# Kernel tuning notes

Hardware: AMD Instinct MI355X
Metric: run time of the kernel (lower is better)

Reference implementation:

```python
import jax, jax.numpy as jnp
import numpy as np

HEADS = 4
DIM_HEAD = 128


def setup_inputs() -> dict:
    key = jax.random.key(0)
    k1, k2, k3, k4 = jax.random.split(key, 4)
    b, dim, H, W = 4, 256, 128, 128
    hidden = HEADS * DIM_HEAD  # 512
    x = jax.random.normal(k1, (b, dim, H, W), dtype=jnp.float32)
    # 1x1 convs are pointwise matmuls over channels
    w_qkv = jax.random.normal(k2, (hidden * 3, dim), dtype=jnp.float32) * 0.02
    w_out = jax.random.normal(k3, (dim, hidden), dtype=jnp.float32) * 0.02
    b_out = jax.random.normal(k4, (dim,), dtype=jnp.float32) * 0.02
    return {"x": x, "w_qkv": w_qkv, "w_out": w_out, "b_out": b_out}


def reference(x, w_qkv, w_out, b_out):
    b, c, h, w = x.shape
    n = h * w
    # to_qkv: 1x1 conv (no bias) == channel matmul -> [b, 3*heads*dh, h, w]
    qkv = jnp.einsum('bchw,oc->bohw', x, w_qkv)
    # 'b (qkv heads d) h w -> qkv b heads d (h w)'
    qkv = qkv.reshape(b, 3, HEADS, DIM_HEAD, n)
    q, k, v = qkv[:, 0], qkv[:, 1], qkv[:, 2]  # each [b, heads, d, n]
    k = jax.nn.softmax(k, axis=-1)  # softmax over spatial positions
    context = jnp.einsum('bhdn,bhen->bhde', k, v)   # [b, heads, d, d]
    out = jnp.einsum('bhde,bhdn->bhen', context, q)  # [b, heads, d, n]
    out = out.reshape(b, HEADS * DIM_HEAD, h, w)
    # to_out: 1x1 conv with bias
    return jnp.einsum('bchw,oc->bohw', out, w_out) + b_out[None, :, None, None]
```

## Files before the change

kernel.cpp:

```cpp
#include <hip/hip_runtime.h>
#include <hip/hip_bf16.h>

#define HEADS 4
#define DH    128
#define CIN   256
#define NPIX  16384
#define NB    4
#define HID   512

typedef __attribute__((ext_vector_type(8))) short bf16x8;
typedef __attribute__((ext_vector_type(4))) float f32x4;
typedef __attribute__((ext_vector_type(2))) unsigned u32x2;

__device__ __forceinline__ unsigned short f2bfu(float f) {
    union { __hip_bfloat16 h; unsigned short u; } cv;
    cv.h = __float2bfloat16(f);
    return cv.u;
}

typedef const __attribute__((address_space(1))) unsigned char* gas_t;
typedef __attribute__((address_space(3))) unsigned char* las_t;
__device__ __forceinline__ void glds16(const void* g, void* s) {
    __builtin_amdgcn_global_load_lds((gas_t)g, (las_t)s, 16, 0, 0);
}
__device__ __forceinline__ unsigned lds_off(const void* p) {
    return (unsigned)(size_t)(las_t)p;
}


__global__ __launch_bounds__(256) void xp_convert(const float* __restrict__ x,
                                                  unsigned short* __restrict__ xp)
{
    __shared__ float tile[64][67];
    const int b = blockIdx.z, c0 = blockIdx.y * 64, n0 = blockIdx.x * 64;
    const int t = threadIdx.x;
    const float* xb = x + ((size_t)b * CIN + c0) * NPIX + n0;
#pragma unroll
    for (int p = 0; p < 4; ++p) {
        const int c = p * 16 + (t >> 4);
        const int n = (t & 15) * 4;
        float4 v = *reinterpret_cast<const float4*>(xb + (size_t)c * NPIX + n);
        tile[c][n + 0] = v.x; tile[c][n + 1] = v.y;
        tile[c][n + 2] = v.z; tile[c][n + 3] = v.w;
    }
    __syncthreads();
    const int n16l = t >> 6, c16l = (t >> 4) & 3, n_loc = t & 15;
    unsigned short u16[16];
#pragma unroll
    for (int j = 0; j < 16; ++j)
        u16[j] = f2bfu(tile[c16l * 16 + j][n16l * 16 + n_loc]);
    unsigned short* dst = xp + (((size_t)(b * 1024 + (n0 >> 4) + n16l)) * 16
                                + (c0 >> 4) + c16l) * 256 + n_loc * 16;
    *reinterpret_cast<uint4*>(dst)     = *reinterpret_cast<const uint4*>(u16);
    *reinterpret_cast<uint4*>(dst + 8) = *reinterpret_cast<const uint4*>(u16 + 8);
}

__global__ __launch_bounds__(256) void wconv3(const float* __restrict__ w_qkv,
                                              const float* __restrict__ w_out,
                                              unsigned short* __restrict__ WkF,
                                              unsigned short* __restrict__ WvF,
                                              unsigned short* __restrict__ WqTF,
                                              unsigned short* __restrict__ WoF)
{
    const int t = threadIdx.x, lane = t & 63, wid = t >> 6;
    const int tile = blockIdx.x * 4 + wid;
    unsigned short u8[8];
    unsigned short* dst;
    if (tile < 256) {
        const int h = tile >> 6, d16 = (tile >> 3) & 7, c32 = tile & 7;
        const float* src = w_qkv + (size_t)(512 + h * 128 + d16 * 16 + (lane & 15)) * CIN
                         + c32 * 32 + (lane >> 4) * 8;
#pragma unroll
        for (int j = 0; j < 8; ++j) u8[j] = f2bfu(src[j]);
        dst = WkF + (size_t)tile * 512 + lane * 8;
    } else if (tile < 512) {
        const int t2 = tile - 256;
        const int h = t2 >> 6, e16 = (t2 >> 3) & 7, c32 = t2 & 7;
        const float* src = w_qkv + (size_t)(1024 + h * 128 + e16 * 16 + (lane & 15)) * CIN
                         + c32 * 32 + (lane >> 4) * 8;
#pragma unroll
        for (int j = 0; j < 8; ++j) u8[j] = f2bfu(src[j]);
        dst = WvF + (size_t)t2 * 512 + lane * 8;
    } else if (tile < 768) {
        const int t2 = tile - 512;
        const int h = t2 >> 6, c16 = (t2 >> 2) & 15, d32 = t2 & 3;
#pragma unroll
        for (int j = 0; j < 8; ++j)
            u8[j] = f2bfu(w_qkv[(size_t)(h * 128 + d32 * 32 + (lane >> 4) * 8 + j) * CIN
                                + c16 * 16 + (lane & 15)]);
        dst = WqTF + (size_t)t2 * 512 + lane * 8;
    } else {
        const int t2 = tile - 768;
        const int o16 = t2 >> 4, m32 = t2 & 15;
        const float* src = w_out + (size_t)(o16 * 16 + (lane & 15)) * HID
                         + m32 * 32 + (lane >> 4) * 8;
#pragma unroll
        for (int j = 0; j < 8; ++j) u8[j] = f2bfu(src[j]);
        dst = WoF + (size_t)t2 * 512 + lane * 8;
    }
    *reinterpret_cast<uint4*>(dst) = *reinterpret_cast<const uint4*>(u8);
}

__global__ __launch_bounds__(512, 2) void kg_fused7(const unsigned short* __restrict__ xp,
                                                    const unsigned short* __restrict__ WkF,
                                                    float* __restrict__ Gp,
                                                    float* __restrict__ S)
{
    __shared__ unsigned short sX[2][64 * 256];
    __shared__ unsigned short sP[16 * 512];

    const int wgid = blockIdx.x;
    const int xcd  = wgid & 7;
    const int k_   = wgid >> 3;
    const int h    = k_ & 3;
    const int g_   = xcd + 8 * (k_ >> 2);
    const int ns   = g_ & 15;
    const int b    = g_ >> 4;
    const int bh   = b * 4 + h;

    const int t = threadIdx.x, lane = t & 63, wid = t >> 6;
    const int wm = wid >> 1, wn = wid & 1;
    const int wd = wid >> 2, wcq = wid & 3;
    const int cl = lane & 15, q = lane >> 4, r0q = q * 4;
    const int boff  = cl * 16 + (q & 1) * 8 + (q >> 1) * 256;
    const unsigned troff = (unsigned)((q >> 1) * 8192 + (q & 1) * 256 + cl * 8);

    bf16x8 aW[2][8];
#pragma unroll
    for (int fi = 0; fi < 2; ++fi)
#pragma unroll
        for (int ks = 0; ks < 8; ++ks)
            aW[fi][ks] = *reinterpret_cast<const bf16x8*>(
                WkF + ((size_t)(h * 64 + (wm * 2 + fi) * 8 + ks)) * 512 + lane * 8);

    f32x4 accG[4][4] = {};
    float Sacc[8] = {};

    const unsigned short* xpb = xp + ((size_t)(b * 1024 + ns * 64) * 16) * 256;

#define STAGE(nt_, buf_)                                                        \
    {                                                                           \
        const unsigned short* src_ = xpb + (size_t)(nt_) * 16384;               \
        _Pragma("unroll")                                                       \
        for (int p = 0; p < 4; ++p)                                             \
            glds16(src_ + ((size_t)p * 512 + t) * 8,                            \
                   &sX[buf_][((size_t)p * 512 + wid * 64) * 8]);                \
    }

    STAGE(0, 0);
    __syncthreads();

    int cur = 0;
    for (int nt = 0; nt < 16; ++nt) {
        if (nt < 15) STAGE(nt + 1, cur ^ 1);

        f32x4 acc1[2][2] = {};
#pragma unroll
        for (int ks = 0; ks < 8; ++ks) {
            bf16x8 bb[2];
#pragma unroll
            for (int fj = 0; fj < 2; ++fj)
                bb[fj] = *reinterpret_cast<const bf16x8*>(
                    &sX[cur][((wn * 2 + fj) * 16 + 2 * ks) * 256 + boff]);
#pragma unroll
            for (int fi = 0; fi < 2; ++fi)
#pragma unroll
                for (int fj = 0; fj < 2; ++fj)
                    acc1[fi][fj] = __builtin_amdgcn_mfma_f32_16x16x32_bf16(
                        aW[fi][ks], bb[fj], acc1[fi][fj], 0, 0, 0);
        }

#pragma unroll
        for (int fi = 0; fi < 2; ++fi)
#pragma unroll
            for (int r = 0; r < 4; ++r) {
                float rs = 0.f;
#pragma unroll
                for (int fj = 0; fj < 2; ++fj) {
                    const float v = __expf(acc1[fi][fj][r]);
                    rs += v;
                    const int us = ((r0q + r) + 16 * (fj * 2 + (cl >> 3))) * 8 + (cl & 7);
                    sP[((wm * 2 + fi) * 2 + wn) * 512 + us] = f2bfu(v);
                }
                Sacc[fi * 4 + r] += rs;
            }
        __syncthreads();

        {
            const unsigned sx_base = lds_off(&sX[cur][0]);
#pragma unroll
            for (int kn = 0; kn < 2; ++kn) {
                u32x2 lo[4], hi[4];
#pragma unroll
                for (int fj = 0; fj < 4; ++fj) {
                    const int cc = wcq * 4 + fj;
                    const unsigned a = sx_base + (unsigned)((kn * 32 + cc) * 512) + troff;
                    asm volatile("ds_read_b64_tr_b16 %0, %2\n\t"
                                 "ds_read_b64_tr_b16 %1, %2 offset:128"
                                 : "=&v"(lo[fj]), "=&v"(hi[fj])
                                 : "v"(a));
                }
                asm volatile("s_waitcnt lgkmcnt(0)" ::: "memory");
                __builtin_amdgcn_sched_barrier(0);

                bf16x8 pa[4];
#pragma unroll
                for (int fi = 0; fi < 4; ++fi)
                    pa[fi] = *reinterpret_cast<const bf16x8*>(
                        &sP[((wd * 4 + fi) * 2 + kn) * 512 + lane * 8]);
#pragma unroll
                for (int fj = 0; fj < 4; ++fj) {
                    union { bf16x8 v; u32x2 h2[2]; } fb;
                    fb.h2[0] = lo[fj];
                    fb.h2[1] = hi[fj];
#pragma unroll
                    for (int fi = 0; fi < 4; ++fi)
                        accG[fi][fj] = __builtin_amdgcn_mfma_f32_16x16x32_bf16(
                            pa[fi], fb.v, accG[fi][fj], 0, 0, 0);
                }
            }
        }
        __syncthreads();
        cur ^= 1;
    }
#undef STAGE

#pragma unroll
    for (int i = 0; i < 8; ++i) {
        float v = Sacc[i];
        v += __shfl_xor(v, 1); v += __shfl_xor(v, 2);
        v += __shfl_xor(v, 4); v += __shfl_xor(v, 8);
        if (cl == 0) {
            const int d = wm * 32 + (i >> 2) * 16 + r0q + (i & 3);
            atomicAdd(&S[bh * 128 + d], v);
        }
    }

    float* gp = Gp + (size_t)(ns * 16 + bh) * (128 * 256);
#pragma unroll
    for (int fi = 0; fi < 4; ++fi)
#pragma unroll
        for (int fj = 0; fj < 4; ++fj)
#pragma unroll
            for (int r = 0; r < 4; ++r)
                gp[(size_t)(wd * 64 + fi * 16 + r0q + r) * 256 + wcq * 64 + fj * 16 + cl]
                    = accG[fi][fj][r];
}

__global__ __launch_bounds__(256) void g_reduce2(const float* __restrict__ Gp,
                                                 float* __restrict__ G)
{
    const int idx = blockIdx.x * 256 + threadIdx.x;
    const int bh = idx >> 15, dc = idx & 32767;
    float s = 0.f;
#pragma unroll
    for (int k = 0; k < 16; ++k)
        s += Gp[((size_t)k * 16 + bh) * 32768 + dc];
    G[idx] = s;
}

__global__ __launch_bounds__(256) void c1_kernel(const float* __restrict__ G,
                                                 const float* __restrict__ S,
                                                 const unsigned short* __restrict__ WvF,
                                                 const unsigned short* __restrict__ WqTF,
                                                 unsigned short* __restrict__ AbarF)
{
    __shared__ unsigned short sCtx[32 * 512];
    const int t = threadIdx.x, lane = t & 63, wid = t >> 6;
    const int bh = blockIdx.x, b = bh >> 2, h = bh & 3;
    const int cl = lane & 15, r0q = (lane >> 4) * 4;
    const int wr = wid >> 1, wc = wid & 1;
    const float* Gb = G + (size_t)bh * 32768;

    float invs[4];
#pragma unroll
    for (int fi = 0; fi < 4; ++fi)
        invs[fi] = 1.0f / S[bh * 128 + wr * 64 + fi * 16 + cl];

    f32x4 acc[4][4] = {};
#pragma unroll
    for (int ks = 0; ks < 8; ++ks) {
        bf16x8 a[4], bb[4];
#pragma unroll
        for (int fi = 0; fi < 4; ++fi) {
            const float* gp = Gb + (size_t)(wr * 64 + fi * 16 + cl) * 256
                            + ks * 32 + (lane >> 4) * 8;
            const float4 v0 = *reinterpret_cast<const float4*>(gp);
            const float4 v1 = *reinterpret_cast<const float4*>(gp + 4);
            unsigned short u8[8] = {
                f2bfu(v0.x * invs[fi]), f2bfu(v0.y * invs[fi]),
                f2bfu(v0.z * invs[fi]), f2bfu(v0.w * invs[fi]),
                f2bfu(v1.x * invs[fi]), f2bfu(v1.y * invs[fi]),
                f2bfu(v1.z * invs[fi]), f2bfu(v1.w * invs[fi]) };
            a[fi] = *reinterpret_cast<const bf16x8*>(u8);
        }
#pragma unroll
        for (int fj = 0; fj < 4; ++fj)
            bb[fj] = *reinterpret_cast<const bf16x8*>(
                WvF + ((size_t)(h * 8 + wc * 4 + fj) * 8 + ks) * 512 + lane * 8);
#pragma unroll
        for (int fi = 0; fi < 4; ++fi)
#pragma unroll
            for (int fj = 0; fj < 4; ++fj)
                acc[fi][fj] = __builtin_amdgcn_mfma_f32_16x16x32_bf16(
                    a[fi], bb[fj], acc[fi][fj], 0, 0, 0);
    }

#pragma unroll
    for (int fi = 0; fi < 4; ++fi)
#pragma unroll
        for (int fj = 0; fj < 4; ++fj)
#pragma unroll
            for (int r = 0; r < 4; ++r) {
                const int us = (cl + 16 * ((fi & 1) * 2 + ((r0q + r) >> 3))) * 8 + ((r0q + r) & 7);
                sCtx[((wc * 4 + fj) * 4 + wr * 2 + (fi >> 1)) * 512 + us] = f2bfu(acc[fi][fj][r]);
            }
    __syncthreads();

    const int we = wid >> 1, wcq = wid & 1;
    f32x4 acc2[4][8] = {};
#pragma unroll
    for (int ks = 0; ks < 4; ++ks) {
        bf16x8 a2[4], b2[8];
#pragma unroll
        for (int fi = 0; fi < 4; ++fi)
            a2[fi] = *reinterpret_cast<const bf16x8*>(
                &sCtx[((we * 4 + fi) * 4 + ks) * 512 + lane * 8]);
#pragma unroll
        for (int fj = 0; fj < 8; ++fj)
            b2[fj] = *reinterpret_cast<const bf16x8*>(
                WqTF + ((size_t)(h * 16 + wcq * 8 + fj) * 4 + ks) * 512 + lane * 8);
#pragma unroll
        for (int fi = 0; fi < 4; ++fi)
#pragma unroll
            for (int fj = 0; fj < 8; ++fj)
                acc2[fi][fj] = __builtin_amdgcn_mfma_f32_16x16x32_bf16(
                    a2[fi], b2[fj], acc2[fi][fj], 0, 0, 0);
    }

#pragma unroll
    for (int fi = 0; fi < 4; ++fi)
#pragma unroll
        for (int fj = 0; fj < 8; ++fj)
#pragma unroll
            for (int r = 0; r < 4; ++r) {
                const int c16 = wcq * 8 + fj;
                const int m32 = h * 4 + we * 2 + (fi >> 1);
                const int us  = (cl + 16 * ((fi & 1) * 2 + ((r0q + r) >> 3))) * 8 + ((r0q + r) & 7);
                AbarF[((size_t)(b * 16 + c16) * 16 + m32) * 512 + us] = f2bfu(acc2[fi][fj][r]);
            }
}

__global__ __launch_bounds__(256) void c2_kernel(const unsigned short* __restrict__ WoF,
                                                 const unsigned short* __restrict__ AbarF,
                                                 unsigned short* __restrict__ F2)
{
    const int t = threadIdx.x, lane = t & 63, wid = t >> 6;
    const int csp = blockIdx.x, b = blockIdx.y;
    const int cl = lane & 15, r0q = (lane >> 4) * 4;

    f32x4 acc[4][4] = {};
#pragma unroll
    for (int ks = 0; ks < 16; ++ks) {
        bf16x8 a[4], bb[4];
#pragma unroll
        for (int fi = 0; fi < 4; ++fi)
            a[fi] = *reinterpret_cast<const bf16x8*>(
                WoF + ((size_t)(wid * 4 + fi) * 16 + ks) * 512 + lane * 8);
#pragma unroll
        for (int fj = 0; fj < 4; ++fj)
            bb[fj] = *reinterpret_cast<const bf16x8*>(
                AbarF + ((size_t)(b * 16 + csp * 4 + fj) * 16 + ks) * 512 + lane * 8);
#pragma unroll
        for (int fi = 0; fi < 4; ++fi)
#pragma unroll
            for (int fj = 0; fj < 4; ++fj)
                acc[fi][fj] = __builtin_amdgcn_mfma_f32_16x16x32_bf16(
                    a[fi], bb[fj], acc[fi][fj], 0, 0, 0);
    }

#pragma unroll
    for (int fi = 0; fi < 4; ++fi)
#pragma unroll
        for (int fj = 0; fj < 4; ++fj)
#pragma unroll
            for (int r = 0; r < 4; ++r) {
                const int o16 = wid * 4 + fi;
                const int c32 = csp * 2 + (fj >> 1);
                const int us  = ((r0q + r) + 16 * ((fj & 1) * 2 + (cl >> 3))) * 8 + (cl & 7);
                F2[((size_t)(b * 16 + o16) * 8 + c32) * 512 + us] = f2bfu(acc[fi][fj][r]);
            }
}

__global__ __launch_bounds__(256, 2) void out_gemm4(const unsigned short* __restrict__ xp,
                                                    const unsigned short* __restrict__ F2,
                                                    const float* __restrict__ b_out,
                                                    float* __restrict__ out)
{
    __shared__ unsigned short sXT[128 * 256];
    const int t = threadIdx.x, lane = t & 63, wid = t >> 6;
    const int n0 = blockIdx.x * 128, m0 = blockIdx.y * 128, b = blockIdx.z;
    const int wr = wid >> 1, wc = wid & 1;
    const int cl = lane & 15, q = lane >> 4;
    const int boff = cl * 16 + (q & 1) * 8 + (q >> 1) * 256;

    const unsigned short* src = xp + ((size_t)(b * 1024 + (n0 >> 4)) * 16) * 256;
#pragma unroll
    for (int p = 0; p < 16; ++p)
        glds16(src + ((size_t)p * 256 + t) * 8, &sXT[((size_t)p * 256 + wid * 64) * 8]);
    __syncthreads();

    f32x4 acc[4][4] = {};
#pragma unroll
    for (int ks = 0; ks < 8; ++ks) {
        bf16x8 a[4], bb[4];
#pragma unroll
        for (int fi = 0; fi < 4; ++fi)
            a[fi] = *reinterpret_cast<const bf16x8*>(
                F2 + (((size_t)b * 16 + (m0 >> 4) + wr * 4 + fi) * 8 + ks) * 512 + lane * 8);
#pragma unroll
        for (int fj = 0; fj < 4; ++fj)
            bb[fj] = *reinterpret_cast<const bf16x8*>(
                &sXT[((wc * 4 + fj) * 16 + 2 * ks) * 256 + boff]);
#pragma unroll
        for (int fi = 0; fi < 4; ++fi)
#pragma unroll
            for (int fj = 0; fj < 4; ++fj)
                acc[fi][fj] = __builtin_amdgcn_mfma_f32_16x16x32_bf16(
                    a[fi], bb[fj], acc[fi][fj], 0, 0, 0);
    }

    const int r0q = q * 4;
#pragma unroll
    for (int fi = 0; fi < 4; ++fi)
#pragma unroll
        for (int r = 0; r < 4; ++r) {
            const int o = m0 + wr * 64 + fi * 16 + r0q + r;
            const float bias = b_out[o];
#pragma unroll
            for (int fj = 0; fj < 4; ++fj)
                out[((size_t)b * CIN + o) * NPIX + n0 + wc * 64 + fj * 16 + cl] =
                    acc[fi][fj][r] + bias;
        }
}

extern "C" void kernel_launch(void* const* d_in, const int* in_sizes, int n_in,
                              void* d_out, int out_size, void* d_ws, size_t ws_size,
                              hipStream_t stream)
{
    const float* x     = (const float*)d_in[0];
    const float* w_qkv = (const float*)d_in[1];
    const float* w_out = (const float*)d_in[2];
    const float* b_out = (const float*)d_in[3];
    float* out = (float*)d_out;

    char* ws = (char*)d_ws;
    unsigned short* xp    = (unsigned short*)ws;
    unsigned short* WkF   = (unsigned short*)(ws + (64ull << 20));
    unsigned short* WvF   = (unsigned short*)(ws + (64ull << 20) + (256u << 10));
    unsigned short* WqTF  = (unsigned short*)(ws + (64ull << 20) + (512u << 10));
    unsigned short* WoF   = (unsigned short*)(ws + (64ull << 20) + (768u << 10));
    float*          S     = (float*)(ws + (65ull << 20));
    float*          G     = (float*)(ws + (66ull << 20));
    unsigned short* AbarF = (unsigned short*)(ws + (68ull << 20));
    unsigned short* F2    = (unsigned short*)(ws + (69ull << 20));
    float*          Gp    = (float*)(ws + (72ull << 20));

    hipMemsetAsync(S, 0, 2048 * sizeof(float), stream);
    xp_convert<<<dim3(NPIX / 64, CIN / 64, NB), 256, 0, stream>>>(x, xp);
    wconv3<<<256, 256, 0, stream>>>(w_qkv, w_out, WkF, WvF, WqTF, WoF);
    kg_fused7<<<256, 512, 0, stream>>>(xp, WkF, Gp, S);
    g_reduce2<<<2048, 256, 0, stream>>>(Gp, G);
    c1_kernel<<<16, 256, 0, stream>>>(G, S, WvF, WqTF, AbarF);
    c2_kernel<<<dim3(4, NB), 256, 0, stream>>>(WoF, AbarF, F2);
    out_gemm4<<<dim3(NPIX / 128, CIN / 128, NB), 256, 0, stream>>>(xp, F2, b_out, out);
}
```

Baseline: 127.5 us.

## Split key-context kernel across head-dim halves and store partial contexts in bf16

The fused key-softmax/context kernel now launches 512 blocks of 256 threads. Each block handles half of a head's 128 key dims, which doubles the grid and shrinks per-block register and LDS use. Partial context sums are written as bf16 instead of fp32, halving the traffic for the partial write and the reduction read. In exchange, each block stages the full x tile, so global-to-LDS loads double, and the bf16 partials lose precision before the 16-way sum.

```diff
diff --git a/kernel.cpp b/kernel.cpp
--- a/kernel.cpp
+++ b/kernel.cpp
@@ -16,6 +16,9 @@
     union { __hip_bfloat16 h; unsigned short u; } cv;
     cv.h = __float2bfloat16(f);
     return cv.u;
+}
+__device__ __forceinline__ float bf2f(unsigned short u) {
+    return __uint_as_float(((unsigned)u) << 16);
 }
 
 typedef const __attribute__((address_space(1))) unsigned char* gas_t;
@@ -101,40 +104,37 @@
     *reinterpret_cast<uint4*>(dst) = *reinterpret_cast<const uint4*>(u8);
 }
 
-__global__ __launch_bounds__(512, 2) void kg_fused7(const unsigned short* __restrict__ xp,
+__global__ __launch_bounds__(256, 2) void kg_fused8(const unsigned short* __restrict__ xp,
                                                     const unsigned short* __restrict__ WkF,
-                                                    float* __restrict__ Gp,
+                                                    unsigned short* __restrict__ Gp,
                                                     float* __restrict__ S)
 {
     __shared__ unsigned short sX[2][64 * 256];
-    __shared__ unsigned short sP[16 * 512];
+    __shared__ unsigned short sP[8 * 512];
 
     const int wgid = blockIdx.x;
     const int xcd  = wgid & 7;
     const int k_   = wgid >> 3;
-    const int h    = k_ & 3;
-    const int g_   = xcd + 8 * (k_ >> 2);
-    const int ns   = g_ & 15;
-    const int b    = g_ >> 4;
-    const int bh   = b * 4 + h;
-
-    const int t = threadIdx.x, lane = t & 63, wid = t >> 6;
-    const int wm = wid >> 1, wn = wid & 1;
-    const int wd = wid >> 2, wcq = wid & 3;
+    const int hd   = k_ & 7;
+    const int gg   = k_ >> 3;
+    const int h = hd >> 1, dh = hd & 1;
+    const int g = xcd + 8 * gg;
+    const int ns = g & 15, b = g >> 4;
+    const int bh = b * 4 + h;
+
+    const int t = threadIdx.x, lane = t & 63, w = t >> 6;
     const int cl = lane & 15, q = lane >> 4, r0q = q * 4;
-    const int boff  = cl * 16 + (q & 1) * 8 + (q >> 1) * 256;
+    const int boff = cl * 16 + (q & 1) * 8 + (q >> 1) * 256;
     const unsigned troff = (unsigned)((q >> 1) * 8192 + (q & 1) * 256 + cl * 8);
 
-    bf16x8 aW[2][8];
-#pragma unroll
-    for (int fi = 0; fi < 2; ++fi)
-#pragma unroll
-        for (int ks = 0; ks < 8; ++ks)
-            aW[fi][ks] = *reinterpret_cast<const bf16x8*>(
-                WkF + ((size_t)(h * 64 + (wm * 2 + fi) * 8 + ks)) * 512 + lane * 8);
+    bf16x8 aW[8];
+#pragma unroll
+    for (int ks = 0; ks < 8; ++ks)
+        aW[ks] = *reinterpret_cast<const bf16x8*>(
+            WkF + ((size_t)((h * 8 + dh * 4 + w) * 8 + ks)) * 512 + lane * 8);
 
     f32x4 accG[4][4] = {};
-    float Sacc[8] = {};
+    float Sacc[4] = {};
 
     const unsigned short* xpb = xp + ((size_t)(b * 1024 + ns * 64) * 16) * 256;
 
@@ -142,9 +142,9 @@
     {                                                                           \
         const unsigned short* src_ = xpb + (size_t)(nt_) * 16384;               \
         _Pragma("unroll")                                                       \
-        for (int p = 0; p < 4; ++p)                                             \
-            glds16(src_ + ((size_t)p * 512 + t) * 8,                            \
-                   &sX[buf_][((size_t)p * 512 + wid * 64) * 8]);                \
+        for (int p = 0; p < 8; ++p)                                             \
+            glds16(src_ + (size_t)p * 2048 + (size_t)t * 8,                     \
+                   &sX[buf_][(size_t)p * 2048 + (size_t)w * 512]);              \
     }
 
     STAGE(0, 0);
@@ -154,35 +154,28 @@
     for (int nt = 0; nt < 16; ++nt) {
         if (nt < 15) STAGE(nt + 1, cur ^ 1);
 
-        f32x4 acc1[2][2] = {};
+        f32x4 acc1[4] = {};
 #pragma unroll
         for (int ks = 0; ks < 8; ++ks) {
-            bf16x8 bb[2];
-#pragma unroll
-            for (int fj = 0; fj < 2; ++fj)
+            bf16x8 bb[4];
+#pragma unroll
+            for (int fj = 0; fj < 4; ++fj)
                 bb[fj] = *reinterpret_cast<const bf16x8*>(
-                    &sX[cur][((wn * 2 + fj) * 16 + 2 * ks) * 256 + boff]);
-#pragma unroll
-            for (int fi = 0; fi < 2; ++fi)
-#pragma unroll
-                for (int fj = 0; fj < 2; ++fj)
-                    acc1[fi][fj] = __builtin_amdgcn_mfma_f32_16x16x32_bf16(
-                        aW[fi][ks], bb[fj], acc1[fi][fj], 0, 0, 0);
+                    &sX[cur][(fj * 16 + 2 * ks) * 256 + boff]);
+#pragma unroll
+            for (int fj = 0; fj < 4; ++fj)
+                acc1[fj] = __builtin_amdgcn_mfma_f32_16x16x32_bf16(
+                    aW[ks], bb[fj], acc1[fj], 0, 0, 0);
         }
 
 #pragma unroll
-        for (int fi = 0; fi < 2; ++fi)
+        for (int fj = 0; fj < 4; ++fj)
 #pragma unroll
             for (int r = 0; r < 4; ++r) {
-                float rs = 0.f;
-#pragma unroll
-                for (int fj = 0; fj < 2; ++fj) {
-                    const float v = __expf(acc1[fi][fj][r]);
-                    rs += v;
-                    const int us = ((r0q + r) + 16 * (fj * 2 + (cl >> 3))) * 8 + (cl & 7);
-                    sP[((wm * 2 + fi) * 2 + wn) * 512 + us] = f2bfu(v);
-                }
-                Sacc[fi * 4 + r] += rs;
+                const float v = __expf(acc1[fj][r]);
+                Sacc[r] += v;
+                const int us = ((r0q + r) + 16 * ((fj & 1) * 2 + (cl >> 3))) * 8 + (cl & 7);
+                sP[(w * 2 + (fj >> 1)) * 512 + us] = f2bfu(v);
             }
         __syncthreads();
 
@@ -193,7 +186,7 @@
                 u32x2 lo[4], hi[4];
 #pragma unroll
                 for (int fj = 0; fj < 4; ++fj) {
-                    const int cc = wcq * 4 + fj;
+                    const int cc = w * 4 + fj;
                     const unsigned a = sx_base + (unsigned)((kn * 32 + cc) * 512) + troff;
                     asm volatile("ds_read_b64_tr_b16 %0, %2\n\t"
                                  "ds_read_b64_tr_b16 %1, %2 offset:128"
@@ -207,7 +200,7 @@
 #pragma unroll
                 for (int fi = 0; fi < 4; ++fi)
                     pa[fi] = *reinterpret_cast<const bf16x8*>(
-                        &sP[((wd * 4 + fi) * 2 + kn) * 512 + lane * 8]);
+                        &sP[(fi * 2 + kn) * 512 + lane * 8]);
 #pragma unroll
                 for (int fj = 0; fj < 4; ++fj) {
                     union { bf16x8 v; u32x2 h2[2]; } fb;
@@ -226,28 +219,26 @@
 #undef STAGE
 
 #pragma unroll
-    for (int i = 0; i < 8; ++i) {
-        float v = Sacc[i];
+    for (int r = 0; r < 4; ++r) {
+        float v = Sacc[r];
         v += __shfl_xor(v, 1); v += __shfl_xor(v, 2);
         v += __shfl_xor(v, 4); v += __shfl_xor(v, 8);
-        if (cl == 0) {
-            const int d = wm * 32 + (i >> 2) * 16 + r0q + (i & 3);
-            atomicAdd(&S[bh * 128 + d], v);
-        }
-    }
-
-    float* gp = Gp + (size_t)(ns * 16 + bh) * (128 * 256);
+        if (cl == 0)
+            atomicAdd(&S[bh * 128 + dh * 64 + w * 16 + r0q + r], v);
+    }
+
+    unsigned short* gp = Gp + (size_t)(ns * 16 + bh) * 32768;
 #pragma unroll
     for (int fi = 0; fi < 4; ++fi)
 #pragma unroll
         for (int fj = 0; fj < 4; ++fj)
 #pragma unroll
             for (int r = 0; r < 4; ++r)
-                gp[(size_t)(wd * 64 + fi * 16 + r0q + r) * 256 + wcq * 64 + fj * 16 + cl]
-                    = accG[fi][fj][r];
-}
-
-__global__ __launch_bounds__(256) void g_reduce2(const float* __restrict__ Gp,
+                gp[(size_t)(dh * 64 + fi * 16 + r0q + r) * 256 + w * 64 + fj * 16 + cl]
+                    = f2bfu(accG[fi][fj][r]);
+}
+
+__global__ __launch_bounds__(256) void g_reduce2(const unsigned short* __restrict__ Gp,
                                                  float* __restrict__ G)
 {
     const int idx = blockIdx.x * 256 + threadIdx.x;
@@ -255,7 +246,7 @@
     float s = 0.f;
 #pragma unroll
     for (int k = 0; k < 16; ++k)
-        s += Gp[((size_t)k * 16 + bh) * 32768 + dc];
+        s += bf2f(Gp[((size_t)k * 16 + bh) * 32768 + dc]);
     G[idx] = s;
 }
 
@@ -464,12 +455,12 @@
     float*          G     = (float*)(ws + (66ull << 20));
     unsigned short* AbarF = (unsigned short*)(ws + (68ull << 20));
     unsigned short* F2    = (unsigned short*)(ws + (69ull << 20));
-    float*          Gp    = (float*)(ws + (72ull << 20));
+    unsigned short* Gp    = (unsigned short*)(ws + (72ull << 20));
 
     hipMemsetAsync(S, 0, 2048 * sizeof(float), stream);
     xp_convert<<<dim3(NPIX / 64, CIN / 64, NB), 256, 0, stream>>>(x, xp);
     wconv3<<<256, 256, 0, stream>>>(w_qkv, w_out, WkF, WvF, WqTF, WoF);
-    kg_fused7<<<256, 512, 0, stream>>>(xp, WkF, Gp, S);
+    kg_fused8<<<512, 256, 0, stream>>>(xp, WkF, Gp, S);
     g_reduce2<<<2048, 256, 0, stream>>>(Gp, G);
     c1_kernel<<<16, 256, 0, stream>>>(G, S, WvF, WqTF, AbarF);
     c2_kernel<<<dim3(4, NB), 256, 0, stream>>>(WoF, AbarF, F2);
```

Result: faster. 121.9 us (-4.4%).
